# Performance work log

Hardware: AMD Instinct MI355X
Metric: run time of the kernel (lower is better)

Reference implementation:

```python
import jax, jax.numpy as jnp
import numpy as np

B, T, D = 2, 2048, 1024
N_HEAD = 16
D_HEAD = D // N_HEAD


def setup_inputs() -> dict:
    key = jax.random.key(0)
    k1, k2, k3 = jax.random.split(key, 3)
    x = jax.random.normal(k1, (B, T, D), dtype=jnp.float32)
    # torch nn.Linear stores weight as [out, in]; we store [in, out] for x @ W
    w_qkv = jax.random.normal(k2, (D, 3 * D), dtype=jnp.float32) * (D ** -0.5)
    w_proj = jax.random.normal(k3, (D, D), dtype=jnp.float32) * (D ** -0.5)
    return {"x": x, "w_qkv": w_qkv, "w_proj": w_proj}


def reference(x, w_qkv, w_proj):
    Bx, Tx, Cx = x.shape
    qkv = (x @ w_qkv).reshape(Bx, Tx, 3, N_HEAD, D_HEAD)
    qkv = jnp.transpose(qkv, (2, 0, 3, 1, 4))  # [3, B, H, T, d]
    q, k, v = qkv[0], qkv[1], qkv[2]
    scale = D_HEAD ** -0.5
    att = jnp.einsum('bhqd,bhkd->bhqk', q, k) * scale  # [B,H,T,T]
    causal = jnp.tril(jnp.ones((Tx, Tx), dtype=bool))
    att = jnp.where(causal, att, -jnp.inf)
    att = jax.nn.softmax(att, axis=-1)
    # dropout p=0.0 -> identity
    y = jnp.einsum('bhqk,bhkd->bhqd', att, v)
    y = jnp.transpose(y, (0, 2, 1, 3)).reshape(Bx, Tx, Cx)
    return y @ w_proj
```

## Files before the change

kernel.cpp:

```cpp
#include <hip/hip_runtime.h>
#include <hip/hip_bf16.h>


typedef __attribute__((ext_vector_type(8))) short bf16x8;
typedef __attribute__((ext_vector_type(4))) float f32x4;

__device__ __forceinline__ ushort f2bf(float f) {
  unsigned u = __builtin_bit_cast(unsigned, f);
  unsigned r = (u + 0x7fffu + ((u >> 16) & 1u)) >> 16;
  return (ushort)r;
}
__device__ __forceinline__ float bf2f(ushort u) {
  unsigned v = ((unsigned)u) << 16;
  return __builtin_bit_cast(float, v);
}
__device__ __forceinline__ unsigned cvtpk(float a, float b) {
  unsigned r;
  asm("v_cvt_pk_bf16_f32 %0, %1, %2" : "=v"(r) : "v"(a), "v"(b));
  return r;
}

__device__ __forceinline__ void gload16(const ushort* g, ushort* l) {
  auto gp = (const __attribute__((address_space(1))) void*)g;
  auto lp = (__attribute__((address_space(3))) void*)l;
  __builtin_amdgcn_global_load_lds(gp, lp, 16, 0, 0);
}

__device__ __forceinline__ int nch2_of(int a) {
  if (a >= 8) return (a + 2) >> 1;
  if (a >= 4) return 2;
  return 1;
}

__global__ __launch_bounds__(256) void prep(const float* __restrict__ x,
                                            const float* __restrict__ wq,
                                            const float* __restrict__ wp,
                                            ushort* __restrict__ xb,
                                            ushort* __restrict__ wqT,
                                            ushort* __restrict__ wpT) {
  __shared__ float tile[32][33];
  const int bx = blockIdx.x;
  if (bx < 4096) {
    int i = (bx * 256 + threadIdx.x) * 4;
    float4 v = *(const float4*)(x + i);
    ushort4 o = { f2bf(v.x), f2bf(v.y), f2bf(v.z), f2bf(v.w) };
    *(ushort4*)(xb + i) = o;
    return;
  }
  const float* in;  ushort* out;  int C, b2;
  if (bx < 7168) { b2 = bx - 4096; in = wq; out = wqT; C = 3072; }
  else           { b2 = bx - 7168; in = wp; out = wpT; C = 1024; }
  const int R = 1024;
  int nbx = C / 32;
  int c0 = (b2 % nbx) * 32, r0 = (b2 / nbx) * 32;
  int tx = threadIdx.x & 31, ty = threadIdx.x >> 5;
  #pragma unroll
  for (int i = 0; i < 32; i += 8) tile[ty + i][tx] = in[(size_t)(r0 + ty + i) * C + c0 + tx];
  __syncthreads();
  if (threadIdx.x < 128) {
    int cr = threadIdx.x >> 2, m = threadIdx.x & 3;
    ushort vals[8];
    #pragma unroll
    for (int e = 0; e < 8; e++) vals[e] = f2bf(tile[8 * m + e][cr]);
    *(uint4*)&out[(size_t)(c0 + cr) * R + r0 + 8 * m] = *(uint4*)vals;
  }
}

template <int EPI, int BN>
__global__ __launch_bounds__(256) void gemm_bf16(const ushort* __restrict__ A,
                                                 const ushort* __restrict__ BT,
                                                 ushort* __restrict__ qo, ushort* __restrict__ ko,
                                                 ushort* __restrict__ vo, float* __restrict__ outf,
                                                 int M, int N, int K) {
  constexpr int NB = BN / 32;
  constexpr int ABU = 128 * 32 + BN * 32;
  constexpr int SHU = (EPI == 0 && 2 * 128 * 72 > ABU) ? 2 * 128 * 72 : ABU;
  __shared__ ushort sh[SHU];
  ushort* Als = sh;
  ushort* Bls = sh + 128 * 32;
  const int tid = threadIdx.x;
  const int lane = tid & 63;
  const int w = tid >> 6;
  const int wr = w >> 1, wc = w & 1;
  const int fr = lane & 15, fq = lane >> 4;
  const int flat = blockIdx.x;
  const int cpx = (32 * (N / BN)) >> 3;
  const int swz = (flat & 7) * cpx + (flat >> 3);
  const int bm0 = (swz & 31) * 128;
  const int bn0 = (swz >> 5) * BN;
  const int srow = lane >> 2;
  const int scol = (lane & 3) * 8;

  f32x4 acc[4][NB];
  #pragma unroll
  for (int m = 0; m < 4; m++)
    #pragma unroll
    for (int n = 0; n < NB; n++) acc[m][n] = (f32x4){0.f, 0.f, 0.f, 0.f};

  for (int k0 = 0; k0 < K; k0 += 32) {
    __syncthreads();
    #pragma unroll
    for (int c = 0; c < 2; c++) {
      int chunk = w * 2 + c;
      int rr = chunk * 16 + srow;
      gload16(&A[(size_t)(bm0 + rr) * K + k0 + scol], &Als[chunk * 512]);
    }
    #pragma unroll
    for (int c = 0; c < BN / 64; c++) {
      int chunk = w * (BN / 64) + c;
      int rr = chunk * 16 + srow;
      gload16(&BT[(size_t)(bn0 + rr) * K + k0 + scol], &Bls[chunk * 512]);
    }
    __syncthreads();
    bf16x8 a[4], b[NB];
    #pragma unroll
    for (int m = 0; m < 4; m++) a[m] = *(bf16x8*)&Als[(wr * 64 + m * 16 + fr) * 32 + fq * 8];
    #pragma unroll
    for (int n = 0; n < NB; n++) b[n] = *(bf16x8*)&Bls[(wc * (BN / 2) + n * 16 + fr) * 32 + fq * 8];
    __builtin_amdgcn_s_setprio(1);
    #pragma unroll
    for (int m = 0; m < 4; m++)
      #pragma unroll
      for (int n = 0; n < NB; n++)
        acc[m][n] = __builtin_amdgcn_mfma_f32_16x16x32_bf16(a[m], b[n], acc[m][n], 0, 0, 0);
    __builtin_amdgcn_s_setprio(0);
  }

  if (EPI == 0) {
    __syncthreads();
    ushort* vst = sh;
    #pragma unroll
    for (int m = 0; m < 4; m++)
      #pragma unroll
      for (int n = 0; n < NB; n++)
        #pragma unroll
        for (int jj = 0; jj < 4; jj++) {
          int lt = wr * 64 + m * 16 + fq * 4 + jj;
          int dd = n * 16 + fr;
          vst[(wc * 128 + lt) * 72 + dd] = f2bf(acc[m][n][jj]);
        }
    __syncthreads();
    const int b_ = bm0 >> 11, t0loc = bm0 & 2047;
    const int which = bn0 >> 10;
    const int hbase = (bn0 & 1023) >> 6;
    if (which < 2) {
      ushort* dst = (which == 0) ? qo : ko;
      #pragma unroll
      for (int p = 0; p < 8; p++) {
        int idx = tid + p * 256;
        int hh = idx >> 10, lt = (idx >> 3) & 127, c8 = (idx & 7) * 8;
        uint4 v = *(uint4*)&vst[(hh * 128 + lt) * 72 + c8];
        size_t bh = (size_t)(b_ * 16 + hbase + hh);
        *(uint4*)&dst[(bh * 2048 + t0loc + lt) * 64 + c8] = v;
      }
    } else {
      #pragma unroll
      for (int p = 0; p < 8; p++) {
        int idx = tid + p * 256;
        int hh = idx >> 10, d = (idx >> 4) & 63, m = idx & 15;
        ushort vals[8];
        #pragma unroll
        for (int e = 0; e < 8; e++) vals[e] = vst[(hh * 128 + 16 * e + m) * 72 + d];
        size_t bh = (size_t)(b_ * 16 + hbase + hh);
        *(uint4*)&vo[(bh * 64 + d) * 2048 + t0loc + 8 * m] = *(uint4*)vals;
      }
    }
  } else {
    #pragma unroll
    for (int m = 0; m < 4; m++)
      #pragma unroll
      for (int n = 0; n < NB; n++)
        #pragma unroll
        for (int jj = 0; jj < 4; jj++) {
          int r = bm0 + wr * 64 + m * 16 + fq * 4 + jj;
          int c = bn0 + wc * (BN / 2) + n * 16 + fr;
          outf[(size_t)r * N + c] = acc[m][n][jj];
        }
  }
}

__global__ __launch_bounds__(256, 2) void attn_fwd(const ushort* __restrict__ qg,
                                                   const ushort* __restrict__ kg,
                                                   const ushort* __restrict__ vtg,
                                                   ushort* __restrict__ y,
                                                   ushort* __restrict__ pO,
                                                   float* __restrict__ pl) {
  __shared__ ushort Ks[128 * 72];
  __shared__ ushort Vt[64 * 136];
  __shared__ ushort Ps[4][32 * 136];

  const int bh = blockIdx.x & 31;
  const int i = blockIdx.x >> 5;
  int acc = 0, a = 15, nch = 1;
  for (int q = 15; q >= 0; --q) {
    int nc = nch2_of(q);
    if (i < acc + nc) { a = q; nch = nc; break; }
    acc += nc;
  }
  const int ch = i - acc;
  const int k = a + 1;
  const int ct = (a >= 8) ? 2 : 4;
  const int t0 = ch * ct;
  const int t1 = (t0 + ct < k) ? t0 + ct : k;

  const int tid = threadIdx.x, lane = tid & 63, w = tid >> 6;
  const int fr = lane & 15, fq = lane >> 4;
  const size_t base = (size_t)bh * 2048 * 64;
  const int b_ = bh >> 4, h = bh & 15;
  const int qb0 = a * 128;
  ushort* P_ = Ps[w];

  const int sr = tid >> 3;
  const int sc = (tid & 7) * 8;
  const int vr = tid >> 4;
  const int vc = (tid & 15) * 8;
  const ushort* kg_l = kg + base + (size_t)sr * 64 + sc;
  const ushort* vg_l = vtg + base + (size_t)vr * 2048 + vc;

  bf16x8 qf[2][2];
  #pragma unroll
  for (int g = 0; g < 2; g++) {
    const ushort* qp = &qg[base + (size_t)(qb0 + w * 32 + g * 16 + fr) * 64];
    qf[g][0] = *(const bf16x8*)(qp + fq * 8);
    qf[g][1] = *(const bf16x8*)(qp + 32 + fq * 8);
  }

  f32x4 o[2][4];
  #pragma unroll
  for (int g = 0; g < 2; g++)
    #pragma unroll
    for (int n = 0; n < 4; n++) o[g][n] = (f32x4){0.f, 0.f, 0.f, 0.f};
  float l_[2][4] = {{0.f,0.f,0.f,0.f},{0.f,0.f,0.f,0.f}};

  uint4 k0r, k1r, k2r, k3r, v0r, v1r, v2r, v3r;

#define LOADT(t)                                                   \
  do {                                                             \
    const ushort* kp = kg_l + (size_t)(t) * 8192;                  \
    k0r = *(const uint4*)(kp);         k1r = *(const uint4*)(kp + 2048); \
    k2r = *(const uint4*)(kp + 4096);  k3r = *(const uint4*)(kp + 6144); \
    const ushort* vp = vg_l + (size_t)(t) * 128;                   \
    v0r = *(const uint4*)(vp);              v1r = *(const uint4*)(vp + 16 * 2048); \
    v2r = *(const uint4*)(vp + 32 * 2048);  v3r = *(const uint4*)(vp + 48 * 2048); \
  } while (0)

  const float C_EXP2 = 0.18033688011112042f;

  LOADT(t0);
  for (int t = t0; t < t1; ++t) {
    const int kv0 = t * 128;
    if (t > t0) __syncthreads();
    *(uint4*)&Ks[(size_t)sr * 72 + sc] = k0r;
    *(uint4*)&Ks[(size_t)(sr + 32) * 72 + sc] = k1r;
    *(uint4*)&Ks[(size_t)(sr + 64) * 72 + sc] = k2r;
    *(uint4*)&Ks[(size_t)(sr + 96) * 72 + sc] = k3r;
    *(uint4*)&Vt[(size_t)vr * 136 + vc] = v0r;
    *(uint4*)&Vt[(size_t)(vr + 16) * 136 + vc] = v1r;
    *(uint4*)&Vt[(size_t)(vr + 32) * 136 + vc] = v2r;
    *(uint4*)&Vt[(size_t)(vr + 48) * 136 + vc] = v3r;
    __syncthreads();

    if (t + 1 < t1) LOADT(t + 1);

    f32x4 s[2][8];
    #pragma unroll
    for (int g = 0; g < 2; g++)
      #pragma unroll
      for (int n = 0; n < 8; n++) s[g][n] = (f32x4){0.f, 0.f, 0.f, 0.f};
    __builtin_amdgcn_s_setprio(1);
    #pragma unroll
    for (int ks = 0; ks < 2; ks++)
      #pragma unroll
      for (int n = 0; n < 8; n++) {
        bf16x8 bk = *(bf16x8*)&Ks[(n * 16 + fr) * 72 + ks * 32 + fq * 8];
        s[0][n] = __builtin_amdgcn_mfma_f32_16x16x32_bf16(qf[0][ks], bk, s[0][n], 0, 0, 0);
        s[1][n] = __builtin_amdgcn_mfma_f32_16x16x32_bf16(qf[1][ks], bk, s[1][n], 0, 0, 0);
      }
    __builtin_amdgcn_s_setprio(0);

    const bool lastT = (t == k - 1);
    #pragma unroll
    for (int g = 0; g < 2; g++)
      #pragma unroll
      for (int j = 0; j < 4; j++) {
        const int qrow = qb0 + w * 32 + g * 16 + fq * 4 + j;
        float p[8];
        float rs = 0.f;
        #pragma unroll
        for (int n = 0; n < 8; n++) {
          float val = s[g][n][j] * C_EXP2;
          if (lastT && (kv0 + n * 16 + fr > qrow)) val = -1e30f;
          p[n] = __builtin_amdgcn_exp2f(val);
          rs += p[n];
        }
        l_[g][j] += rs;
        uint4 pk;
        pk.x = cvtpk(p[0], p[1]);
        pk.y = cvtpk(p[2], p[3]);
        pk.z = cvtpk(p[4], p[5]);
        pk.w = cvtpk(p[6], p[7]);
        *(uint4*)&P_[(g * 16 + fq * 4 + j) * 136 + 8 * fr] = pk;
      }

    __builtin_amdgcn_s_setprio(1);
    #pragma unroll
    for (int ks = 0; ks < 4; ks++) {
      bf16x8 pa0 = *(bf16x8*)&P_[fr * 136 + ks * 32 + fq * 8];
      bf16x8 pa1 = *(bf16x8*)&P_[(16 + fr) * 136 + ks * 32 + fq * 8];
      #pragma unroll
      for (int n2 = 0; n2 < 4; n2++) {
        bf16x8 vb8 = *(bf16x8*)&Vt[(n2 * 16 + fr) * 136 + ks * 32 + fq * 8];
        o[0][n2] = __builtin_amdgcn_mfma_f32_16x16x32_bf16(pa0, vb8, o[0][n2], 0, 0, 0);
        o[1][n2] = __builtin_amdgcn_mfma_f32_16x16x32_bf16(pa1, vb8, o[1][n2], 0, 0, 0);
      }
    }
    __builtin_amdgcn_s_setprio(0);
  }
#undef LOADT

  #pragma unroll
  for (int g = 0; g < 2; g++)
    #pragma unroll
    for (int j = 0; j < 4; j++) {
      float rs = l_[g][j];
      rs += __shfl_xor(rs, 1);
      rs += __shfl_xor(rs, 2);
      rs += __shfl_xor(rs, 4);
      rs += __shfl_xor(rs, 8);
      l_[g][j] = rs;
    }

  if (nch == 1) {
    #pragma unroll
    for (int g = 0; g < 2; g++)
      #pragma unroll
      for (int n2 = 0; n2 < 4; n2++)
        #pragma unroll
        for (int j = 0; j < 4; j++) {
          int qrow = qb0 + w * 32 + g * 16 + fq * 4 + j;
          y[((size_t)(b_ * 2048 + qrow)) * 1024 + h * 64 + n2 * 16 + fr] =
              f2bf(o[g][n2][j] / l_[g][j]);
        }
  } else {
    const size_t ob = ((size_t)i * 32 + bh) * 128 * 64;
    #pragma unroll
    for (int g = 0; g < 2; g++)
      #pragma unroll
      for (int n2 = 0; n2 < 4; n2++)
        #pragma unroll
        for (int j = 0; j < 4; j++) {
          int qr = w * 32 + g * 16 + fq * 4 + j;
          pO[ob + (size_t)qr * 64 + n2 * 16 + fr] = f2bf(o[g][n2][j]);
        }
    if (fr == 0) {
      #pragma unroll
      for (int g = 0; g < 2; g++)
        #pragma unroll
        for (int j = 0; j < 4; j++)
          pl[((size_t)i * 32 + bh) * 128 + w * 32 + g * 16 + fq * 4 + j] = l_[g][j];
    }
  }
}

__global__ __launch_bounds__(256) void attn_combine(const ushort* __restrict__ pO,
                                                    const float* __restrict__ pl,
                                                    ushort* __restrict__ y) {
  int flat = blockIdx.x * 256 + threadIdx.x;
  int d8 = (flat & 7) * 8;
  int ridx = flat >> 3;
  int bh = ridx / 1536;
  int r = ridx - bh * 1536;
  int a = 4 + (r >> 7);
  int tloc = r & 127;
  int t = a * 128 + tloc;
  int nch = nch2_of(a);
  int baseSlot = (a >= 8) ? (71 - ((a * a) >> 2) - a) : (52 + 2 * (7 - a));
  float os0=0.f, os1=0.f, os2=0.f, os3=0.f, os4=0.f, os5=0.f, os6=0.f, os7=0.f;
  float ls = 0.f;
  for (int c = 0; c < nch; ++c) {
    int slot = baseSlot + c;
    uint4 v = *(const uint4*)&pO[((size_t)slot * 32 + bh) * 128 * 64 + (size_t)tloc * 64 + d8];
    os0 += bf2f((ushort)(v.x & 0xffff));  os1 += bf2f((ushort)(v.x >> 16));
    os2 += bf2f((ushort)(v.y & 0xffff));  os3 += bf2f((ushort)(v.y >> 16));
    os4 += bf2f((ushort)(v.z & 0xffff));  os5 += bf2f((ushort)(v.z >> 16));
    os6 += bf2f((ushort)(v.w & 0xffff));  os7 += bf2f((ushort)(v.w >> 16));
    ls += pl[((size_t)slot * 32 + bh) * 128 + tloc];
  }
  float inv = 1.f / ls;
  uint4 o;
  o.x = cvtpk(os0 * inv, os1 * inv);
  o.y = cvtpk(os2 * inv, os3 * inv);
  o.z = cvtpk(os4 * inv, os5 * inv);
  o.w = cvtpk(os6 * inv, os7 * inv);
  int b_ = bh >> 4, h = bh & 15;
  *(uint4*)&y[((size_t)(b_ * 2048 + t)) * 1024 + h * 64 + d8] = o;
}

extern "C" void kernel_launch(void* const* d_in, const int* in_sizes, int n_in,
                              void* d_out, int out_size, void* d_ws, size_t ws_size,
                              hipStream_t stream) {
  const float* x = (const float*)d_in[0];
  const float* wqkv = (const float*)d_in[1];
  const float* wproj = (const float*)d_in[2];
  float* out = (float*)d_out;

  ushort* ws = (ushort*)d_ws;
  ushort* xb = ws;
  ushort* wqkvT = xb + 4096 * 1024;
  ushort* wprojT = wqkvT + 3072 * 1024;
  ushort* qb = wprojT + 1024 * 1024;
  ushort* kb = qb + 32 * 2048 * 64;
  ushort* vtb = kb + 32 * 2048 * 64;
  ushort* yb = vtb + 32 * 2048 * 64;
  ushort* pO = yb + 4096 * 1024;
  float*  pl = (float*)(pO + (size_t)64 * 32 * 128 * 64);

  prep<<<8192, 256, 0, stream>>>(x, wqkv, wproj, xb, wqkvT, wprojT);
  gemm_bf16<0, 128><<<768, 256, 0, stream>>>(xb, wqkvT, qb, kb, vtb, nullptr, 4096, 3072, 1024);
  attn_fwd<<<2048, 256, 0, stream>>>(qb, kb, vtb, yb, pO, pl);
  attn_combine<<<1536, 256, 0, stream>>>(pO, pl, yb);
  gemm_bf16<1, 64><<<512, 256, 0, stream>>>(yb, wprojT, nullptr, nullptr, nullptr, out, 4096, 1024, 1024);
}
```

Baseline: 117.6 us.

## Shrink attention KV tile to 64 keys and permute V-transpose layout to match

```diff
diff --git a/kernel.cpp b/kernel.cpp
--- a/kernel.cpp
+++ b/kernel.cpp
@@ -158,11 +158,13 @@
       for (int p = 0; p < 8; p++) {
         int idx = tid + p * 256;
         int hh = idx >> 10, d = (idx >> 4) & 63, m = idx & 15;
+        int blk = m >> 3, m4 = m & 7;
         ushort vals[8];
         #pragma unroll
-        for (int e = 0; e < 8; e++) vals[e] = vst[(hh * 128 + 16 * e + m) * 72 + d];
+        for (int r = 0; r < 8; r++)
+          vals[r] = vst[(hh * 128 + blk * 64 + 16 * (r & 3) + 2 * m4 + (r >> 2)) * 72 + d];
         size_t bh = (size_t)(b_ * 16 + hbase + hh);
-        *(uint4*)&vo[(bh * 64 + d) * 2048 + t0loc + 8 * m] = *(uint4*)vals;
+        *(uint4*)&vo[(bh * 64 + d) * 2048 + t0loc + blk * 64 + 8 * m4] = *(uint4*)vals;
       }
     }
   } else {
@@ -185,9 +187,9 @@
                                                    ushort* __restrict__ y,
                                                    ushort* __restrict__ pO,
                                                    float* __restrict__ pl) {
-  __shared__ ushort Ks[128 * 72];
-  __shared__ ushort Vt[64 * 136];
-  __shared__ ushort Ps[4][32 * 136];
+  __shared__ ushort Ks[64 * 72];
+  __shared__ ushort Vt[64 * 72];
+  __shared__ ushort Ps[4][32 * 72];
 
   const int bh = blockIdx.x & 31;
   const int i = blockIdx.x >> 5;
@@ -198,10 +200,10 @@
     acc += nc;
   }
   const int ch = i - acc;
-  const int k = a + 1;
-  const int ct = (a >= 8) ? 2 : 4;
+  const int k64 = 2 * (a + 1);
+  const int ct = (a >= 8) ? 4 : 8;
   const int t0 = ch * ct;
-  const int t1 = (t0 + ct < k) ? t0 + ct : k;
+  const int t1 = (t0 + ct < k64) ? t0 + ct : k64;
 
   const int tid = threadIdx.x, lane = tid & 63, w = tid >> 6;
   const int fr = lane & 15, fq = lane >> 4;
@@ -210,12 +212,12 @@
   const int qb0 = a * 128;
   ushort* P_ = Ps[w];
 
-  const int sr = tid >> 3;
-  const int sc = (tid & 7) * 8;
-  const int vr = tid >> 4;
-  const int vc = (tid & 15) * 8;
-  const ushort* kg_l = kg + base + (size_t)sr * 64 + sc;
-  const ushort* vg_l = vtg + base + (size_t)vr * 2048 + vc;
+  const int kr = tid >> 2;
+  const int kc8 = (tid & 3) * 8;
+  const int vr = tid >> 3;
+  const int vc8 = (tid & 7) * 8;
+  const ushort* kg_l = kg + base + (size_t)kr * 64 + kc8;
+  const ushort* vg_l = vtg + base + (size_t)vr * 2048 + vc8;
 
   bf16x8 qf[2][2];
   #pragma unroll
@@ -232,84 +234,84 @@
     for (int n = 0; n < 4; n++) o[g][n] = (f32x4){0.f, 0.f, 0.f, 0.f};
   float l_[2][4] = {{0.f,0.f,0.f,0.f},{0.f,0.f,0.f,0.f}};
 
-  uint4 k0r, k1r, k2r, k3r, v0r, v1r, v2r, v3r;
-
-#define LOADT(t)                                                   \
-  do {                                                             \
-    const ushort* kp = kg_l + (size_t)(t) * 8192;                  \
-    k0r = *(const uint4*)(kp);         k1r = *(const uint4*)(kp + 2048); \
-    k2r = *(const uint4*)(kp + 4096);  k3r = *(const uint4*)(kp + 6144); \
-    const ushort* vp = vg_l + (size_t)(t) * 128;                   \
-    v0r = *(const uint4*)(vp);              v1r = *(const uint4*)(vp + 16 * 2048); \
-    v2r = *(const uint4*)(vp + 32 * 2048);  v3r = *(const uint4*)(vp + 48 * 2048); \
+  uint4 k0r, k1r, v0r, v1r;
+
+#define LOADT(t)                                              \
+  do {                                                        \
+    const ushort* kp = kg_l + (size_t)(t) * 4096;             \
+    k0r = *(const uint4*)(kp);                                \
+    k1r = *(const uint4*)(kp + 32);                           \
+    const ushort* vp = vg_l + (size_t)(t) * 64;               \
+    v0r = *(const uint4*)(vp);                                \
+    v1r = *(const uint4*)(vp + 32 * 2048);                    \
   } while (0)
 
   const float C_EXP2 = 0.18033688011112042f;
 
   LOADT(t0);
   for (int t = t0; t < t1; ++t) {
-    const int kv0 = t * 128;
+    const int kv0 = t * 64;
     if (t > t0) __syncthreads();
-    *(uint4*)&Ks[(size_t)sr * 72 + sc] = k0r;
-    *(uint4*)&Ks[(size_t)(sr + 32) * 72 + sc] = k1r;
-    *(uint4*)&Ks[(size_t)(sr + 64) * 72 + sc] = k2r;
-    *(uint4*)&Ks[(size_t)(sr + 96) * 72 + sc] = k3r;
-    *(uint4*)&Vt[(size_t)vr * 136 + vc] = v0r;
-    *(uint4*)&Vt[(size_t)(vr + 16) * 136 + vc] = v1r;
-    *(uint4*)&Vt[(size_t)(vr + 32) * 136 + vc] = v2r;
-    *(uint4*)&Vt[(size_t)(vr + 48) * 136 + vc] = v3r;
+    *(uint4*)&Ks[(size_t)kr * 72 + kc8] = k0r;
+    *(uint4*)&Ks[(size_t)kr * 72 + kc8 + 32] = k1r;
+    *(uint4*)&Vt[(size_t)vr * 72 + vc8] = v0r;
+    *(uint4*)&Vt[(size_t)(vr + 32) * 72 + vc8] = v1r;
     __syncthreads();
 
     if (t + 1 < t1) LOADT(t + 1);
 
-    f32x4 s[2][8];
+    f32x4 s[2][4];
     #pragma unroll
     for (int g = 0; g < 2; g++)
       #pragma unroll
-      for (int n = 0; n < 8; n++) s[g][n] = (f32x4){0.f, 0.f, 0.f, 0.f};
+      for (int n = 0; n < 4; n++) s[g][n] = (f32x4){0.f, 0.f, 0.f, 0.f};
     __builtin_amdgcn_s_setprio(1);
     #pragma unroll
     for (int ks = 0; ks < 2; ks++)
       #pragma unroll
-      for (int n = 0; n < 8; n++) {
+      for (int n = 0; n < 4; n++) {
         bf16x8 bk = *(bf16x8*)&Ks[(n * 16 + fr) * 72 + ks * 32 + fq * 8];
         s[0][n] = __builtin_amdgcn_mfma_f32_16x16x32_bf16(qf[0][ks], bk, s[0][n], 0, 0, 0);
         s[1][n] = __builtin_amdgcn_mfma_f32_16x16x32_bf16(qf[1][ks], bk, s[1][n], 0, 0, 0);
       }
     __builtin_amdgcn_s_setprio(0);
 
-    const bool lastT = (t == k - 1);
+    const bool maskT = (t >= k64 - 2);
     #pragma unroll
     for (int g = 0; g < 2; g++)
       #pragma unroll
       for (int j = 0; j < 4; j++) {
         const int qrow = qb0 + w * 32 + g * 16 + fq * 4 + j;
-        float p[8];
-        float rs = 0.f;
-        #pragma unroll
-        for (int n = 0; n < 8; n++) {
-          float val = s[g][n][j] * C_EXP2;
-          if (lastT && (kv0 + n * 16 + fr > qrow)) val = -1e30f;
-          p[n] = __builtin_amdgcn_exp2f(val);
-          rs += p[n];
+        float p0, p1, p2, p3;
+        {
+          float v0 = s[g][0][j] * C_EXP2, v1 = s[g][1][j] * C_EXP2;
+          float v2 = s[g][2][j] * C_EXP2, v3 = s[g][3][j] * C_EXP2;
+          if (maskT) {
+            if (kv0 +  0 + fr > qrow) v0 = -1e30f;
+            if (kv0 + 16 + fr > qrow) v1 = -1e30f;
+            if (kv0 + 32 + fr > qrow) v2 = -1e30f;
+            if (kv0 + 48 + fr > qrow) v3 = -1e30f;
+          }
+          p0 = __builtin_amdgcn_exp2f(v0);
+          p1 = __builtin_amdgcn_exp2f(v1);
+          p2 = __builtin_amdgcn_exp2f(v2);
+          p3 = __builtin_amdgcn_exp2f(v3);
         }
-        l_[g][j] += rs;
-        uint4 pk;
-        pk.x = cvtpk(p[0], p[1]);
-        pk.y = cvtpk(p[2], p[3]);
-        pk.z = cvtpk(p[4], p[5]);
-        pk.w = cvtpk(p[6], p[7]);
-        *(uint4*)&P_[(g * 16 + fq * 4 + j) * 136 + 8 * fr] = pk;
+        l_[g][j] += (p0 + p1) + (p2 + p3);
+        uint2 pk;
+        pk.x = cvtpk(p0, p1);
+        pk.y = cvtpk(p2, p3);
+        *(uint2*)&P_[(g * 16 + fq * 4 + j) * 72 + 4 * fr] = pk;
       }
 
     __builtin_amdgcn_s_setprio(1);
     #pragma unroll
-    for (int ks = 0; ks < 4; ks++) {
-      bf16x8 pa0 = *(bf16x8*)&P_[fr * 136 + ks * 32 + fq * 8];
-      bf16x8 pa1 = *(bf16x8*)&P_[(16 + fr) * 136 + ks * 32 + fq * 8];
+    for (int ks = 0; ks < 2; ks++) {
+      bf16x8 pa0 = *(bf16x8*)&P_[fr * 72 + ks * 32 + fq * 8];
+      bf16x8 pa1 = *(bf16x8*)&P_[(16 + fr) * 72 + ks * 32 + fq * 8];
       #pragma unroll
       for (int n2 = 0; n2 < 4; n2++) {
-        bf16x8 vb8 = *(bf16x8*)&Vt[(n2 * 16 + fr) * 136 + ks * 32 + fq * 8];
+        bf16x8 vb8 = *(bf16x8*)&Vt[(n2 * 16 + fr) * 72 + ks * 32 + fq * 8];
         o[0][n2] = __builtin_amdgcn_mfma_f32_16x16x32_bf16(pa0, vb8, o[0][n2], 0, 0, 0);
         o[1][n2] = __builtin_amdgcn_mfma_f32_16x16x32_bf16(pa1, vb8, o[1][n2], 0, 0, 0);
       }
```

Result: faster. 115.2 us (-2.1%).
